# Optimization experiments

Measured on AMD Instinct MI355X. Metric: run time of the kernel, lower is better.

Reference implementation:

```python
import jax, jax.numpy as jnp
import numpy as np

VOCAB = 65
N_EMBD = 32
HEAD = 16
BLOCK = 8
B = 65536


def setup_inputs() -> dict:
    key = jax.random.key(0)
    ks = jax.random.split(key, 12)
    idx = jax.random.randint(ks[0], (B, BLOCK), 0, VOCAB)
    targets = jax.random.randint(ks[1], (B, BLOCK), 0, VOCAB)
    s = 0.02
    tok_emb = jax.random.normal(ks[2], (VOCAB, N_EMBD), jnp.float32) * s
    pos_emb = jax.random.normal(ks[3], (BLOCK, N_EMBD), jnp.float32) * s
    Wk = jax.random.normal(ks[4], (N_EMBD, HEAD), jnp.float32) * s
    bk = jnp.zeros((HEAD,), jnp.float32)
    Wq = jax.random.normal(ks[5], (N_EMBD, HEAD), jnp.float32) * s
    bq = jnp.zeros((HEAD,), jnp.float32)
    Wv = jax.random.normal(ks[6], (N_EMBD, HEAD), jnp.float32) * s
    bv = jnp.zeros((HEAD,), jnp.float32)
    Wlm = jax.random.normal(ks[7], (HEAD, VOCAB), jnp.float32) * s
    blm = jnp.zeros((VOCAB,), jnp.float32)
    return {"idx": idx, "targets": targets, "tok_emb": tok_emb, "pos_emb": pos_emb,
            "Wk": Wk, "bk": bk, "Wq": Wq, "bq": bq, "Wv": Wv, "bv": bv,
            "Wlm": Wlm, "blm": blm}


def reference(idx, targets, tok_emb, pos_emb, Wk, bk, Wq, bq, Wv, bv, Wlm, blm):
    Bsz, T = idx.shape
    x = tok_emb[idx] + pos_emb[None, :T, :]                  # (B,T,C)
    k = x @ Wk + bk                                          # (B,T,H)
    q = x @ Wq + bq
    wei = jnp.einsum('bth,bsh->bts', q, k) * (HEAD ** -0.5)  # (B,T,T)
    tril = jnp.tril(jnp.ones((T, T), bool))
    wei = jnp.where(tril[None], wei, -jnp.inf)
    # NOTE: original torch code uses F.softmax(wei, dim=1) — over the QUERY axis.
    wei = jax.nn.softmax(wei, axis=1)
    v = x @ Wv + bv
    attn = jnp.einsum('bts,bsh->bth', wei, v)                # (B,T,H)
    logits = attn @ Wlm + blm                                # (B,T,V)
    logits_flat = logits.reshape(Bsz * T, VOCAB)
    tgt_flat = targets.reshape(Bsz * T)
    logp = jax.nn.log_softmax(logits_flat, axis=-1)
    loss = -jnp.mean(jnp.take_along_axis(logp, tgt_flat[:, None], axis=-1))
    return logits_flat, loss
```

## Files before the change

kernel.cpp:

```cpp
#include <hip/hip_runtime.h>

#define NVOC 65
#define NE   32
#define HD   16
#define NB   65536
#define NROWS (NB * 8)
#define NLOG  (NROWS * NVOC)


static __device__ __forceinline__ float readlane_f(float v, int l) {
  return __uint_as_float(__builtin_amdgcn_readlane(__float_as_uint(v), l));
}

__global__ __launch_bounds__(1024) void bigram_tables(
    const float* __restrict__ tok, const float* __restrict__ pos,
    const float* __restrict__ Wk, const float* __restrict__ bk,
    const float* __restrict__ Wq, const float* __restrict__ bq,
    const float* __restrict__ Wv, const float* __restrict__ bv,
    const float* __restrict__ Wlm, float* __restrict__ ws)
{
  __shared__ float S[8416];
  const int tid = threadIdx.x;
  for (int o = tid; o < 2080; o += 1024) S[o] = tok[o];
  for (int o = tid; o < 256;  o += 1024) S[2080 + o] = pos[o];
  for (int o = tid; o < 512;  o += 1024) {
    S[2336 + o] = Wq[o]; S[2848 + o] = Wk[o]; S[3360 + o] = Wv[o];
  }
  for (int o = tid; o < 1040; o += 1024) S[3872 + o] = Wlm[o];
  __syncthreads();

  for (int o = tid; o < 1168; o += 1024) {
    if (o < 1040) {
      const int a = o >> 4, h = o & 15;
      float sq = 0.f, sk = 0.f, sv = 0.f;
      #pragma unroll
      for (int c = 0; c < NE; ++c) {
        const float e = S[a*32 + c];
        sq = fmaf(e, S[2336 + c*16 + h], sq);
        sk = fmaf(e, S[2848 + c*16 + h], sk);
        sv = fmaf(e, S[3360 + c*16 + h], sv);
      }
      S[4912 + o] = sq; S[5952 + o] = sk; S[6992 + o] = sv;
    } else {
      const int o2 = o - 1040, t = o2 >> 4, h = o2 & 15;
      float sq = bq[h], sk = bk[h], sv = bv[h];
      #pragma unroll
      for (int c = 0; c < NE; ++c) {
        const float e = S[2080 + t*32 + c];
        sq = fmaf(e, S[2336 + c*16 + h], sq);
        sk = fmaf(e, S[2848 + c*16 + h], sk);
        sv = fmaf(e, S[3360 + c*16 + h], sv);
      }
      S[8032 + o2] = sq; S[8160 + o2] = sk; S[8288 + o2] = sv;
    }
  }
  __syncthreads();

  float* wsTab = ws + 16;
  for (int o = tid; o < 10074; o += 1024) {
    float r = 0.f; int dst;
    if (o < 4225) {
      const int a = o / 65, b = o % 65;
      #pragma unroll
      for (int h = 0; h < HD; ++h) r = fmaf(S[4912 + a*16 + h], S[5952 + b*16 + h], r);
      r *= 0.25f; dst = o;
    } else if (o < 4745) {
      const int o2 = o - 4225, a = o2 >> 3, s2 = o2 & 7;
      #pragma unroll
      for (int h = 0; h < HD; ++h) r = fmaf(S[4912 + a*16 + h], S[8160 + s2*16 + h], r);
      r *= 0.25f; dst = 8450 + o2;
    } else if (o < 5265) {
      const int o2 = o - 4745, t2 = o2 / 65, b = o2 % 65;
      #pragma unroll
      for (int h = 0; h < HD; ++h) r = fmaf(S[8032 + t2*16 + h], S[5952 + b*16 + h], r);
      r *= 0.25f; dst = 8970 + o2;
    } else if (o < 5329) {
      const int o2 = o - 5265, t2 = o2 >> 3, s2 = o2 & 7;
      #pragma unroll
      for (int h = 0; h < HD; ++h) r = fmaf(S[8032 + t2*16 + h], S[8160 + s2*16 + h], r);
      r *= 0.25f; dst = 9490 + o2;
    } else if (o < 9554) {
      const int o2 = o - 5329, a = o2 / 65, j = o2 % 65;
      #pragma unroll
      for (int h = 0; h < HD; ++h) r = fmaf(S[6992 + a*16 + h], S[3872 + h*65 + j], r);
      dst = 4225 + o2;
    } else {
      const int o2 = o - 9554, s2 = o2 / 65, j = o2 % 65;
      #pragma unroll
      for (int h = 0; h < HD; ++h) r = fmaf(S[8288 + s2*16 + h], S[3872 + h*65 + j], r);
      dst = o;
    }
    wsTab[dst] = r;
  }
}

__global__ __launch_bounds__(512, 8) void bigram_main(
    const int* __restrict__ idx, const int* __restrict__ tgt,
    const float* __restrict__ blm, const float* __restrict__ ws,
    float* __restrict__ wsout, float* __restrict__ out)
{
  __shared__ __align__(16) float S[10074];
  __shared__ float red[8];
  const int tid = threadIdx.x;
  const int lane = tid & 63;
  const int w    = tid >> 6;
  const int t    = lane >> 3;
  const int s    = lane & 7;
  const int u    = lane & 7;
  const int gw = blockIdx.x * 8 + w;
  const int iv = idx[gw*64 + lane];
  const int tv = tgt[gw*64 + lane];
  const float blmj  = blm[lane];
  const float blm64 = blm[64];
  const float* wsTab = ws + 16;
  {
    const float4* t4 = (const float4*)wsTab;
    float4* s4 = (float4*)S;
    for (int o = tid; o < 2518; o += 512) s4[o] = t4[o];
    if (tid < 2) S[10072 + tid] = wsTab[10072 + tid];
  }
  __syncthreads();

  const float g4 = S[9490 + lane];
  float pvl[8], pvl64[8];
  #pragma unroll
  for (int k = 0; k < 8; ++k) {
    pvl[k]   = S[9554 + k*65 + lane];
    pvl64[k] = S[9554 + k*65 + 64];
  }

  float acc_lsm = 0.f, acc_tl = 0.f;
  for (int itb = 0; itb < 8; ++itb) {
    const int base = itb * 8;
    const int av  = __shfl(iv, base + s);
    const int a_t = __shfl(iv, base + t);
    float wr = S[a_t*65 + av] + S[8450 + a_t*8 + s] + S[8970 + t*65 + av] + g4;
    float e = (t >= s) ? __expf(wr) : 0.f;
    float sm = e;
    sm += __shfl_xor(sm, 8); sm += __shfl_xor(sm, 16); sm += __shfl_xor(sm, 32);
    const float wsm = __fdividef(e, sm);
    float Ms[8], Ms64[8];
    #pragma unroll
    for (int k = 0; k < 8; ++k) {
      const int ak = __builtin_amdgcn_readlane(iv, base + k);
      Ms[k]   = S[4225 + ak*65 + lane] + pvl[k];
      Ms64[k] = S[4225 + ak*65 + 64]  + pvl64[k];
    }
    float lg64v = blm64;
    #pragma unroll
    for (int k = 0; k < 8; ++k) {
      const float wk_row = __shfl(wsm, u*8 + k);
      lg64v = fmaf(wk_row, Ms64[k], lg64v);
    }
    const int rowbase = (gw*8 + itb) * 520;
    if (lane < 8) out[rowbase + lane*65 + 64] = lg64v;
    float ee[8];
    #pragma unroll
    for (int tt = 0; tt < 8; ++tt) {
      float lg = blmj;
      #pragma unroll
      for (int k = 0; k < 8; ++k) {
        const float wk = readlane_f(wsm, tt*8 + k);
        lg = fmaf(wk, Ms[k], lg);
      }
      out[rowbase + tt*65 + lane] = lg;
      ee[tt] = __expf(lg);
      const int tg  = __builtin_amdgcn_readlane(tv, base + tt);
      const int tgc = tg < 64 ? tg : 0;
      const float l_at_tg = readlane_f(lg, tgc);
      const float l64t    = readlane_f(lg64v, tt);
      acc_tl += (tg < 64) ? l_at_tg : l64t;
    }
    #pragma unroll
    for (int tt = 0; tt < 8; ++tt) {
      ee[tt] += __shfl_xor(ee[tt], 1);
      ee[tt] += __shfl_xor(ee[tt], 2);
      ee[tt] += __shfl_xor(ee[tt], 4);
    }
    float r01 = (u & 1) ? ee[1] : ee[0];
    float r23 = (u & 1) ? ee[3] : ee[2];
    float r45 = (u & 1) ? ee[5] : ee[4];
    float r67 = (u & 1) ? ee[7] : ee[6];
    float r03 = (u & 2) ? r23 : r01;
    float r47 = (u & 2) ? r67 : r45;
    float r   = (u & 4) ? r47 : r03;
    if (lane < 8) r += __expf(lg64v);
    r += __shfl_xor(r, 8); r += __shfl_xor(r, 16); r += __shfl_xor(r, 32);
    acc_lsm += __logf(r);
  }
  float v = acc_lsm * 0.125f - acc_tl * 0.015625f;
  v += __shfl_xor(v, 1); v += __shfl_xor(v, 2);  v += __shfl_xor(v, 4);
  v += __shfl_xor(v, 8); v += __shfl_xor(v, 16); v += __shfl_xor(v, 32);
  if (lane == 0) red[w] = v;
  __syncthreads();
  if (tid == 0) {
    wsout[10112 + blockIdx.x] = red[0] + red[1] + red[2] + red[3]
                              + red[4] + red[5] + red[6] + red[7];
  }
}

__global__ __launch_bounds__(1024) void bigram_fin2(
    const float* __restrict__ ws, float* __restrict__ out)
{
  __shared__ float r[16];
  const int tid = threadIdx.x;
  float v = ws[10112 + tid];
  v += __shfl_xor(v, 1); v += __shfl_xor(v, 2);  v += __shfl_xor(v, 4);
  v += __shfl_xor(v, 8); v += __shfl_xor(v, 16); v += __shfl_xor(v, 32);
  if ((tid & 63) == 0) r[tid >> 6] = v;
  __syncthreads();
  if (tid == 0) {
    float a = 0.f;
    #pragma unroll
    for (int i = 0; i < 16; ++i) a += r[i];
    out[NLOG] = a * (1.0f / (float)NROWS);
  }
}

extern "C" void kernel_launch(void* const* d_in, const int* in_sizes, int n_in,
                              void* d_out, int out_size, void* d_ws, size_t ws_size,
                              hipStream_t stream) {
  const int* idx = (const int*)d_in[0];
  const int* tgt = (const int*)d_in[1];
  float* ws = (float*)d_ws;
  float* out = (float*)d_out;

  bigram_tables<<<1, 1024, 0, stream>>>((const float*)d_in[2], (const float*)d_in[3],
                                        (const float*)d_in[4], (const float*)d_in[5],
                                        (const float*)d_in[6], (const float*)d_in[7],
                                        (const float*)d_in[8], (const float*)d_in[9],
                                        (const float*)d_in[10], ws);
  bigram_main<<<1024, 512, 0, stream>>>(idx, tgt, (const float*)d_in[11], ws, ws, out);
  bigram_fin2<<<1, 1024, 0, stream>>>(ws, out);
}
```

Before: 200.7 us.

## Split table kernel across blocks, fuse final reduction via atomics, trim causal FMAs

The table-building kernel now runs on 16 blocks, each computing a slice of the output tables while redundantly staging the small weights into shared memory. The separate final-reduction kernel is removed: each main block atomically adds its partial loss, and the last block to finish (tracked by an atomic counter) writes the mean. The inner logits loop skips causally-masked zero weights, the exp-sum reduction uses a transposed butterfly with fewer shuffles, and log is replaced by log2 with a scale. These changes aim to cut a kernel launch, the serial single-block setup, and per-row shuffle and FMA count, at the cost of atomic contention and a float-atomic summation order that is no longer deterministic.

```diff
diff --git a/kernel.cpp b/kernel.cpp
--- a/kernel.cpp
+++ b/kernel.cpp
@@ -21,6 +21,11 @@
 {
   __shared__ float S[8416];
   const int tid = threadIdx.x;
+  const int bid = blockIdx.x;
+  if (bid == 0 && tid == 0) {
+    ws[0] = 0.f;
+    ((unsigned int*)ws)[1] = 0u;
+  }
   for (int o = tid; o < 2080; o += 1024) S[o] = tok[o];
   for (int o = tid; o < 256;  o += 1024) S[2080 + o] = pos[o];
   for (int o = tid; o < 512;  o += 1024) {
@@ -57,7 +62,9 @@
   __syncthreads();
 
   float* wsTab = ws + 16;
-  for (int o = tid; o < 10074; o += 1024) {
+  const int lo = bid * 632;
+  const int hi = (lo + 632 < 10074) ? lo + 632 : 10074;
+  for (int o = lo + tid; o < hi; o += 1024) {
     float r = 0.f; int dst;
     if (o < 4225) {
       const int a = o / 65, b = o % 65;
@@ -96,8 +103,8 @@
 
 __global__ __launch_bounds__(512, 8) void bigram_main(
     const int* __restrict__ idx, const int* __restrict__ tgt,
-    const float* __restrict__ blm, const float* __restrict__ ws,
-    float* __restrict__ wsout, float* __restrict__ out)
+    const float* __restrict__ blm, float* __restrict__ ws,
+    float* __restrict__ out)
 {
   __shared__ __align__(16) float S[10074];
   __shared__ float red[8];
@@ -128,6 +135,7 @@
     pvl[k]   = S[9554 + k*65 + lane];
     pvl64[k] = S[9554 + k*65 + 64];
   }
+  const bool b0 = (lane & 1) != 0, b1 = (lane & 2) != 0, b2 = (lane & 4) != 0;
 
   float acc_lsm = 0.f, acc_tl = 0.f;
   for (int itb = 0; itb < 8; ++itb) {
@@ -159,7 +167,7 @@
     for (int tt = 0; tt < 8; ++tt) {
       float lg = blmj;
       #pragma unroll
-      for (int k = 0; k < 8; ++k) {
+      for (int k = 0; k <= tt; ++k) {
         const float wk = readlane_f(wsm, tt*8 + k);
         lg = fmaf(wk, Ms[k], lg);
       }
@@ -171,49 +179,36 @@
       const float l64t    = readlane_f(lg64v, tt);
       acc_tl += (tg < 64) ? l_at_tg : l64t;
     }
-    #pragma unroll
-    for (int tt = 0; tt < 8; ++tt) {
-      ee[tt] += __shfl_xor(ee[tt], 1);
-      ee[tt] += __shfl_xor(ee[tt], 2);
-      ee[tt] += __shfl_xor(ee[tt], 4);
-    }
-    float r01 = (u & 1) ? ee[1] : ee[0];
-    float r23 = (u & 1) ? ee[3] : ee[2];
-    float r45 = (u & 1) ? ee[5] : ee[4];
-    float r67 = (u & 1) ? ee[7] : ee[6];
-    float r03 = (u & 2) ? r23 : r01;
-    float r47 = (u & 2) ? r67 : r45;
-    float r   = (u & 4) ? r47 : r03;
+    float k0 = b0 ? ee[1] : ee[0], s0 = b0 ? ee[0] : ee[1];
+    float k1 = b0 ? ee[3] : ee[2], s1 = b0 ? ee[2] : ee[3];
+    float k2 = b0 ? ee[5] : ee[4], s2 = b0 ? ee[4] : ee[5];
+    float k3 = b0 ? ee[7] : ee[6], s3 = b0 ? ee[6] : ee[7];
+    k0 += __shfl_xor(s0, 1); k1 += __shfl_xor(s1, 1);
+    k2 += __shfl_xor(s2, 1); k3 += __shfl_xor(s3, 1);
+    float m0 = b1 ? k1 : k0, t0 = b1 ? k0 : k1;
+    float m1 = b1 ? k3 : k2, t1 = b1 ? k2 : k3;
+    m0 += __shfl_xor(t0, 2); m1 += __shfl_xor(t1, 2);
+    float r = b2 ? m1 : m0,  t2 = b2 ? m0 : m1;
+    r += __shfl_xor(t2, 4);
     if (lane < 8) r += __expf(lg64v);
     r += __shfl_xor(r, 8); r += __shfl_xor(r, 16); r += __shfl_xor(r, 32);
-    acc_lsm += __logf(r);
-  }
-  float v = acc_lsm * 0.125f - acc_tl * 0.015625f;
+    acc_lsm += __log2f(r);
+  }
+  float v = acc_lsm * (0.6931471805599453f * 0.125f) - acc_tl * 0.015625f;
   v += __shfl_xor(v, 1); v += __shfl_xor(v, 2);  v += __shfl_xor(v, 4);
   v += __shfl_xor(v, 8); v += __shfl_xor(v, 16); v += __shfl_xor(v, 32);
   if (lane == 0) red[w] = v;
   __syncthreads();
   if (tid == 0) {
-    wsout[10112 + blockIdx.x] = red[0] + red[1] + red[2] + red[3]
-                              + red[4] + red[5] + red[6] + red[7];
-  }
-}
-
-__global__ __launch_bounds__(1024) void bigram_fin2(
-    const float* __restrict__ ws, float* __restrict__ out)
-{
-  __shared__ float r[16];
-  const int tid = threadIdx.x;
-  float v = ws[10112 + tid];
-  v += __shfl_xor(v, 1); v += __shfl_xor(v, 2);  v += __shfl_xor(v, 4);
-  v += __shfl_xor(v, 8); v += __shfl_xor(v, 16); v += __shfl_xor(v, 32);
-  if ((tid & 63) == 0) r[tid >> 6] = v;
-  __syncthreads();
-  if (tid == 0) {
-    float a = 0.f;
-    #pragma unroll
-    for (int i = 0; i < 16; ++i) a += r[i];
-    out[NLOG] = a * (1.0f / (float)NROWS);
+    const float p = red[0] + red[1] + red[2] + red[3]
+                  + red[4] + red[5] + red[6] + red[7];
+    atomicAdd(&ws[0], p);
+    __threadfence();
+    const unsigned int old = atomicAdd(&((unsigned int*)ws)[1], 1u);
+    if (old == 1023u) {
+      const float tot = atomicAdd(&ws[0], 0.0f);
+      out[NLOG] = tot * (1.0f / (float)NROWS);
+    }
   }
 }
 
@@ -225,11 +220,10 @@
   float* ws = (float*)d_ws;
   float* out = (float*)d_out;
 
-  bigram_tables<<<1, 1024, 0, stream>>>((const float*)d_in[2], (const float*)d_in[3],
-                                        (const float*)d_in[4], (const float*)d_in[5],
-                                        (const float*)d_in[6], (const float*)d_in[7],
-                                        (const float*)d_in[8], (const float*)d_in[9],
-                                        (const float*)d_in[10], ws);
-  bigram_main<<<1024, 512, 0, stream>>>(idx, tgt, (const float*)d_in[11], ws, ws, out);
-  bigram_fin2<<<1, 1024, 0, stream>>>(ws, out);
-}
+  bigram_tables<<<16, 1024, 0, stream>>>((const float*)d_in[2], (const float*)d_in[3],
+                                         (const float*)d_in[4], (const float*)d_in[5],
+                                         (const float*)d_in[6], (const float*)d_in[7],
+                                         (const float*)d_in[8], (const float*)d_in[9],
+                                         (const float*)d_in[10], ws);
+  bigram_main<<<1024, 512, 0, stream>>>(idx, tgt, (const float*)d_in[11], ws, out);
+}
```

New measurement: 225.3 us. 12.2% more time.
